# Performance work log

Measured on AMD Instinct MI355X. Metric: run time of the kernel, lower is better.

The kernel has to match this reference:

```python
import jax, jax.numpy as jnp
import numpy as np

N_NODES = 50000
N_EDGES = 800000
IN_FEATS = 128
OUT_FEATS = 128
HEADS = 2
EW_DIMS = 2
NEG_SLOPE = 0.2


def setup_inputs() -> dict:
    key = jax.random.key(0)
    ks = jax.random.split(key, 8)
    feat = jax.random.normal(ks[0], (N_NODES, IN_FEATS), dtype=jnp.float32)
    e_w = jax.random.uniform(ks[1], (N_EDGES, EW_DIMS), dtype=jnp.float32)
    src = jax.random.randint(ks[2], (N_EDGES,), 0, N_NODES)
    dst = jax.random.randint(ks[3], (N_EDGES,), 0, N_NODES)
    # Learned params: per-head fc weight, attn vectors (xavier-ish scale)
    s = 1.0 / np.sqrt(IN_FEATS)
    W = jax.random.normal(ks[4], (HEADS, OUT_FEATS, IN_FEATS), dtype=jnp.float32) * s
    attn_l = jax.random.normal(ks[5], (HEADS, OUT_FEATS), dtype=jnp.float32) * s
    attn_r = jax.random.normal(ks[6], (HEADS, OUT_FEATS), dtype=jnp.float32) * s
    attn_ew = jax.random.normal(ks[7], (HEADS, EW_DIMS), dtype=jnp.float32)
    return {"feat": feat, "e_w": e_w, "src": src, "dst": dst,
            "W": W, "attn_l": attn_l, "attn_r": attn_r, "attn_ew": attn_ew}


def reference(feat, e_w, src, dst, W, attn_l, attn_r, attn_ew):
    N = feat.shape[0]
    # per-head projection: [N, H, O]
    ft = jnp.einsum('nf,hof->nho', feat, W)
    el = jnp.einsum('nho,ho->nh', ft, attn_l)           # [N, H]
    er = jnp.einsum('nho,ho->nh', ft, attn_r)           # [N, H]
    ew = jnp.einsum('ed,hd->eh', e_w, attn_ew)          # [E, H]
    # u_add_v + edge-weight attention + leaky_relu
    e = jax.nn.leaky_relu(el[src] + er[dst] + ew, NEG_SLOPE)  # [E, H]
    # edge_softmax grouped by destination node (numerically stable)
    emax = jax.ops.segment_max(e, dst, num_segments=N)
    emax = jnp.where(jnp.isfinite(emax), emax, 0.0)
    ee = jnp.exp(e - emax[dst])
    denom = jax.ops.segment_sum(ee, dst, num_segments=N)
    a = ee / jnp.where(denom[dst] > 0, denom[dst], 1.0)       # [E, H]
    # u_mul_e / sum aggregation: [N, H, O]
    m = ft[src] * a[:, :, None]
    rst = jax.ops.segment_sum(m, dst, num_segments=N)
    # residual (Identity since in_feats == out_feats) + elu, then cat heads
    rst = jax.nn.elu(rst + feat[:, None, :])
    return rst.reshape(N, -1)
```

## Files before the change

### kernel.cpp

```cpp
#include <hip/hip_runtime.h>
#include <math.h>

#define NNODES 50000
#define NEDGES 800000
#define INF 128
#define OUTF 128
#define HEADS 2
#define NEG_SLOPE 0.2f

#define CAP 32
#define OVFCAP 32768

__device__ __forceinline__ unsigned short f2bf(float f) {
    unsigned u = __float_as_uint(f);
    unsigned r = (u + 0x7FFFu + ((u >> 16) & 1u)) >> 16;
    return (unsigned short)r;
}
__device__ __forceinline__ float bf2f(unsigned short b) {
    return __uint_as_float((unsigned)b << 16);
}

typedef __attribute__((ext_vector_type(8))) short frag_ab;
typedef __attribute__((ext_vector_type(4))) float frag_cd;

__global__ void init_kernel(int* cursor, int* ovfcnt,
                            const float* __restrict__ W,
                            const float* __restrict__ attn_l,
                            const float* __restrict__ attn_r,
                            unsigned short* __restrict__ Wb,
                            float* __restrict__ wfold, int N) {
    const int b = blockIdx.x, t = threadIdx.x;
    const int cblk = (N + 255) >> 8;
    if (b < cblk) {
        int i = b * 256 + t;
        if (i < N) cursor[i] = 0;
        if (i == 0) *ovfcnt = 0;
        return;
    }
    if (b == cblk) {
        int h = t >> 7, f = t & 127;
        float sl = 0.f, sr = 0.f;
        for (int o = 0; o < 128; ++o) {
            float wv = W[(size_t)(h * 128 + o) * 128 + f];
            sl = fmaf(attn_l[h * 128 + o], wv, sl);
            sr = fmaf(attn_r[h * 128 + o], wv, sr);
        }
        wfold[h * 128 + f] = sl;
        wfold[(2 + h) * 128 + f] = sr;
        return;
    }
    int base = (b - cblk - 1) * 4096 + t * 16;
#pragma unroll
    for (int q = 0; q < 4; ++q) {
        float4 g = *(const float4*)(W + base + q * 4);
        ushort4 v; v.x = f2bf(g.x); v.y = f2bf(g.y); v.z = f2bf(g.z); v.w = f2bf(g.w);
        *(ushort4*)(Wb + base + q * 4) = v;
    }
}

__global__ __launch_bounds__(256) void gemm_mfma(const float* __restrict__ feat,
                                                 const unsigned short* __restrict__ Wb,
                                                 const float* __restrict__ wfold,
                                                 unsigned short* __restrict__ ftb,
                                                 float* __restrict__ el,
                                                 float* __restrict__ er,
                                                 int N) {
    const int t = threadIdx.x;
    const int w = t >> 6, lane = t & 63;
    const int m16 = lane & 15, quad = lane >> 4;
    const int n0 = blockIdx.x * 64;
    const int r = n0 + w * 16 + m16;
    const bool valid = r < N;

    frag_ab af[4];
    float pd[4] = {0.f, 0.f, 0.f, 0.f};
#pragma unroll
    for (int kc = 0; kc < 4; ++kc) {
        const int cc = kc * 32 + quad * 8;
        float4 g0 = make_float4(0.f, 0.f, 0.f, 0.f), g1 = g0;
        if (valid) {
            g0 = *(const float4*)(feat + (size_t)r * INF + cc);
            g1 = *(const float4*)(feat + (size_t)r * INF + cc + 4);
        }
        frag_ab a;
        a[0] = (short)f2bf(g0.x); a[1] = (short)f2bf(g0.y);
        a[2] = (short)f2bf(g0.z); a[3] = (short)f2bf(g0.w);
        a[4] = (short)f2bf(g1.x); a[5] = (short)f2bf(g1.y);
        a[6] = (short)f2bf(g1.z); a[7] = (short)f2bf(g1.w);
        af[kc] = a;
#pragma unroll
        for (int vq = 0; vq < 4; ++vq) {
            float4 w0 = *(const float4*)(wfold + vq * 128 + cc);
            float4 w1 = *(const float4*)(wfold + vq * 128 + cc + 4);
            pd[vq] += g0.x * w0.x + g0.y * w0.y + g0.z * w0.z + g0.w * w0.w
                    + g1.x * w1.x + g1.y * w1.y + g1.z * w1.z + g1.w * w1.w;
        }
    }
#pragma unroll
    for (int m = 16; m < 64; m <<= 1)
#pragma unroll
        for (int vq = 0; vq < 4; ++vq) pd[vq] += __shfl_xor(pd[vq], m, 64);
    if (valid && quad == 0) {
        *(float2*)(el + (size_t)r * 2) = make_float2(pd[0], pd[1]);
        *(float2*)(er + (size_t)r * 2) = make_float2(pd[2], pd[3]);
    }

#pragma unroll
    for (int jt = 0; jt < 4; ++jt) {
        frag_cd acc[4];
#pragma unroll
        for (int nt = 0; nt < 4; ++nt) acc[nt] = frag_cd{0.f, 0.f, 0.f, 0.f};
#pragma unroll
        for (int kc = 0; kc < 4; ++kc) {
#pragma unroll
            for (int nt = 0; nt < 4; ++nt) {
                frag_ab bf = *(const frag_ab*)(Wb + (size_t)(jt * 64 + nt * 16 + m16) * INF
                                               + kc * 32 + quad * 8);
                acc[nt] = __builtin_amdgcn_mfma_f32_16x16x32_bf16(af[kc], bf, acc[nt], 0, 0, 0);
            }
        }
#pragma unroll
        for (int nt = 0; nt < 4; ++nt) {
            const int gj = jt * 64 + nt * 16 + m16;
#pragma unroll
            for (int reg = 0; reg < 4; ++reg) {
                int gm = n0 + w * 16 + quad * 4 + reg;
                if (gm < N) ftb[(size_t)gm * 256 + gj] = f2bf(acc[nt][reg]);
            }
        }
    }
}

__global__ void edge_fused(const float* __restrict__ el, const float* __restrict__ er,
                           const float* __restrict__ e_w, const int* __restrict__ src,
                           const int* __restrict__ dst, const float* __restrict__ attn_ew,
                           int* __restrict__ cursor, int* __restrict__ ovfcnt,
                           uint2* __restrict__ edata, float4* __restrict__ ovf,
                           int E) {
    int e = blockIdx.x * 256 + threadIdx.x;
    if (e >= E) return;
    int s = src[e], d = dst[e];
    float2 ew2 = *(const float2*)(e_w + (size_t)e * 2);
    float2 elv = *(const float2*)(el + (size_t)s * 2);
    float2 erv = *(const float2*)(er + (size_t)d * 2);
    float v0 = elv.x + erv.x + ew2.x * attn_ew[0] + ew2.y * attn_ew[1];
    float v1 = elv.y + erv.y + ew2.x * attn_ew[2] + ew2.y * attn_ew[3];
    v0 = v0 >= 0.f ? v0 : NEG_SLOPE * v0;
    v1 = v1 >= 0.f ? v1 : NEG_SLOPE * v1;
    float ee0 = __expf(v0);
    float ee1 = __expf(v1);
    int pos = atomicAdd(cursor + d, 1);
    if (pos < CAP) {
        unsigned pk = ((unsigned)f2bf(ee1) << 16) | (unsigned)f2bf(ee0);
        edata[(size_t)d * CAP + pos] = make_uint2((unsigned)s, pk);
    } else {
        int o = atomicAdd(ovfcnt, 1);
        if (o < OVFCAP)
            ovf[o] = make_float4(__int_as_float(d), __int_as_float(s), ee0, ee1);
    }
}

__global__ __launch_bounds__(256) void aggregate(const unsigned short* __restrict__ ftb,
                                                 const float* __restrict__ feat,
                                                 const uint2* __restrict__ edata,
                                                 const int* __restrict__ cursor,
                                                 const int* __restrict__ ovfcnt,
                                                 const float4* __restrict__ ovf,
                                                 float* __restrict__ out, int N) {
    const int t = threadIdx.x;
    const int w = t >> 6, l = t & 63;
    const int n = blockIdx.x * 4 + w;
    if (n >= N) return;
    const int c0 = 4 * l;
    const int h = l >> 5;
    const int cnt = cursor[n];
    const int cmain = cnt < CAP ? cnt : CAP;
    const uint2* eb = edata + (size_t)n * CAP;
    const uint2 myrec = eb[l & 31];

    float4 acc = make_float4(0.f, 0.f, 0.f, 0.f);
    float dn = 0.f;
#pragma unroll 4
    for (int i = 0; i < cmain; ++i) {
        unsigned sx = (unsigned)__builtin_amdgcn_readlane((int)myrec.x, i);
        unsigned pk = (unsigned)__builtin_amdgcn_readlane((int)myrec.y, i);
        float a = bf2f((unsigned short)(h ? (pk >> 16) : (pk & 0xFFFFu)));
        const ushort4 v = *(const ushort4*)(ftb + (size_t)sx * 256 + c0);
        dn += a;
        acc.x = fmaf(a, bf2f(v.x), acc.x);
        acc.y = fmaf(a, bf2f(v.y), acc.y);
        acc.z = fmaf(a, bf2f(v.z), acc.z);
        acc.w = fmaf(a, bf2f(v.w), acc.w);
    }
    if (cnt > CAP) {
        int no = *ovfcnt; if (no > OVFCAP) no = OVFCAP;
        for (int i = 0; i < no; ++i) {
            float4 ov = ovf[i];
            if (__float_as_int(ov.x) == n) {
                int s = __float_as_int(ov.y);
                float a = h ? ov.w : ov.z;
                dn += a;
                const ushort4 v = *(const ushort4*)(ftb + (size_t)s * 256 + c0);
                acc.x = fmaf(a, bf2f(v.x), acc.x);
                acc.y = fmaf(a, bf2f(v.y), acc.y);
                acc.z = fmaf(a, bf2f(v.z), acc.z);
                acc.w = fmaf(a, bf2f(v.w), acc.w);
            }
        }
    }
    float inv = dn > 0.f ? 1.0f / dn : 0.f;
    float4 f4 = *(const float4*)(feat + (size_t)n * INF + (c0 & 127));
    float4 r;
    r.x = acc.x * inv + f4.x;
    r.y = acc.y * inv + f4.y;
    r.z = acc.z * inv + f4.z;
    r.w = acc.w * inv + f4.w;
    r.x = r.x > 0.f ? r.x : expm1f(r.x);
    r.y = r.y > 0.f ? r.y : expm1f(r.y);
    r.z = r.z > 0.f ? r.z : expm1f(r.z);
    r.w = r.w > 0.f ? r.w : expm1f(r.w);
    *(float4*)(out + (size_t)n * 256 + c0) = r;
}

extern "C" void kernel_launch(void* const* d_in, const int* in_sizes, int n_in,
                              void* d_out, int out_size, void* d_ws, size_t ws_size,
                              hipStream_t stream) {
    const float* feat    = (const float*)d_in[0];
    const float* e_w     = (const float*)d_in[1];
    const int*   src     = (const int*)d_in[2];
    const int*   dst     = (const int*)d_in[3];
    const float* W       = (const float*)d_in[4];
    const float* attn_l  = (const float*)d_in[5];
    const float* attn_r  = (const float*)d_in[6];
    const float* attn_ew = (const float*)d_in[7];
    float* out = (float*)d_out;

    const int N = in_sizes[0] / INF;
    const int E = in_sizes[2];

    unsigned short* ftb = (unsigned short*)d_ws;
    uint2*  edata  = (uint2*)(ftb + (size_t)N * 256);
    float*  el     = (float*)(edata + (size_t)N * CAP);
    float*  er     = el + (size_t)N * 2;
    float*  wfold  = er + (size_t)N * 2;
    unsigned short* Wb = (unsigned short*)(wfold + 512);
    float4* ovf    = (float4*)(Wb + 32768);
    int*    cursor = (int*)(ovf + OVFCAP);
    int*    ovfcnt = cursor + N;

    const int cblk = (N + 255) / 256;
    init_kernel<<<cblk + 9, 256, 0, stream>>>(cursor, ovfcnt, W, attn_l, attn_r, Wb, wfold, N);

    gemm_mfma<<<(N + 63) / 64, 256, 0, stream>>>(feat, Wb, wfold, ftb, el, er, N);

    edge_fused<<<(E + 255) / 256, 256, 0, stream>>>(el, er, e_w, src, dst, attn_ew,
                                                    cursor, ovfcnt, edata, ovf, E);

    aggregate<<<(N + 3) / 4, 256, 0, stream>>>(ftb, feat, edata, cursor, ovfcnt, ovf, out, N);
}
```

Baseline: 251.3 us.

## Split aggregation edges across half-waves with 16-byte feature loads

```diff
diff --git a/kernel.cpp b/kernel.cpp
--- a/kernel.cpp
+++ b/kernel.cpp
@@ -22,6 +22,7 @@
 
 typedef __attribute__((ext_vector_type(8))) short frag_ab;
 typedef __attribute__((ext_vector_type(4))) float frag_cd;
+typedef __attribute__((ext_vector_type(8))) unsigned short ushort8v;
 
 __global__ void init_kernel(int* cursor, int* ovfcnt,
                             const float* __restrict__ W,
@@ -40,6 +41,7 @@
     if (b == cblk) {
         int h = t >> 7, f = t & 127;
         float sl = 0.f, sr = 0.f;
+#pragma unroll 16
         for (int o = 0; o < 128; ++o) {
             float wv = W[(size_t)(h * 128 + o) * 128 + f];
             sl = fmaf(attn_l[h * 128 + o], wv, sl);
@@ -105,20 +107,25 @@
         *(float2*)(er + (size_t)r * 2) = make_float2(pd[2], pd[3]);
     }
 
-#pragma unroll
+#pragma unroll 1
     for (int jt = 0; jt < 4; ++jt) {
+        frag_ab bfr[16];
+#pragma unroll
+        for (int kc = 0; kc < 4; ++kc)
+#pragma unroll
+            for (int nt = 0; nt < 4; ++nt)
+                bfr[kc * 4 + nt] = *(const frag_ab*)(Wb
+                        + (size_t)(jt * 64 + nt * 16 + m16) * INF + kc * 32 + quad * 8);
+
         frag_cd acc[4];
 #pragma unroll
         for (int nt = 0; nt < 4; ++nt) acc[nt] = frag_cd{0.f, 0.f, 0.f, 0.f};
 #pragma unroll
-        for (int kc = 0; kc < 4; ++kc) {
-#pragma unroll
-            for (int nt = 0; nt < 4; ++nt) {
-                frag_ab bf = *(const frag_ab*)(Wb + (size_t)(jt * 64 + nt * 16 + m16) * INF
-                                               + kc * 32 + quad * 8);
-                acc[nt] = __builtin_amdgcn_mfma_f32_16x16x32_bf16(af[kc], bf, acc[nt], 0, 0, 0);
-            }
-        }
+        for (int kc = 0; kc < 4; ++kc)
+#pragma unroll
+            for (int nt = 0; nt < 4; ++nt)
+                acc[nt] = __builtin_amdgcn_mfma_f32_16x16x32_bf16(af[kc], bfr[kc * 4 + nt],
+                                                                  acc[nt], 0, 0, 0);
 #pragma unroll
         for (int nt = 0; nt < 4; ++nt) {
             const int gj = jt * 64 + nt * 16 + m16;
@@ -171,27 +178,47 @@
     const int w = t >> 6, l = t & 63;
     const int n = blockIdx.x * 4 + w;
     if (n >= N) return;
-    const int c0 = 4 * l;
-    const int h = l >> 5;
+    const int hl = l & 31;
+    const int half = l >> 5;
+    const int c8 = 8 * hl;
+    const int h = hl >> 4;
     const int cnt = cursor[n];
     const int cmain = cnt < CAP ? cnt : CAP;
     const uint2* eb = edata + (size_t)n * CAP;
-    const uint2 myrec = eb[l & 31];
-
-    float4 acc = make_float4(0.f, 0.f, 0.f, 0.f);
+
+    float4 a0 = make_float4(0.f, 0.f, 0.f, 0.f);
+    float4 a1 = make_float4(0.f, 0.f, 0.f, 0.f);
     float dn = 0.f;
+    const int hm = (cmain + 1) >> 1;
 #pragma unroll 4
-    for (int i = 0; i < cmain; ++i) {
-        unsigned sx = (unsigned)__builtin_amdgcn_readlane((int)myrec.x, i);
-        unsigned pk = (unsigned)__builtin_amdgcn_readlane((int)myrec.y, i);
-        float a = bf2f((unsigned short)(h ? (pk >> 16) : (pk & 0xFFFFu)));
-        const ushort4 v = *(const ushort4*)(ftb + (size_t)sx * 256 + c0);
+    for (int i = 0; i < hm; ++i) {
+        const int j = 2 * i + half;
+        const bool vld = j < cmain;
+        uint2 rec = eb[vld ? j : 0];
+        float aw = bf2f((unsigned short)(h ? (rec.y >> 16) : (rec.y & 0xFFFFu)));
+        float a = vld ? aw : 0.f;
+        unsigned su = vld ? rec.x : 0u;
+        ushort8v v = *(const ushort8v*)(ftb + (size_t)su * 256 + c8);
         dn += a;
-        acc.x = fmaf(a, bf2f(v.x), acc.x);
-        acc.y = fmaf(a, bf2f(v.y), acc.y);
-        acc.z = fmaf(a, bf2f(v.z), acc.z);
-        acc.w = fmaf(a, bf2f(v.w), acc.w);
-    }
+        a0.x = fmaf(a, bf2f(v[0]), a0.x);
+        a0.y = fmaf(a, bf2f(v[1]), a0.y);
+        a0.z = fmaf(a, bf2f(v[2]), a0.z);
+        a0.w = fmaf(a, bf2f(v[3]), a0.w);
+        a1.x = fmaf(a, bf2f(v[4]), a1.x);
+        a1.y = fmaf(a, bf2f(v[5]), a1.y);
+        a1.z = fmaf(a, bf2f(v[6]), a1.z);
+        a1.w = fmaf(a, bf2f(v[7]), a1.w);
+    }
+    a0.x += __shfl_xor(a0.x, 32, 64);
+    a0.y += __shfl_xor(a0.y, 32, 64);
+    a0.z += __shfl_xor(a0.z, 32, 64);
+    a0.w += __shfl_xor(a0.w, 32, 64);
+    a1.x += __shfl_xor(a1.x, 32, 64);
+    a1.y += __shfl_xor(a1.y, 32, 64);
+    a1.z += __shfl_xor(a1.z, 32, 64);
+    a1.w += __shfl_xor(a1.w, 32, 64);
+    dn += __shfl_xor(dn, 32, 64);
+
     if (cnt > CAP) {
         int no = *ovfcnt; if (no > OVFCAP) no = OVFCAP;
         for (int i = 0; i < no; ++i) {
@@ -200,26 +227,32 @@
                 int s = __float_as_int(ov.y);
                 float a = h ? ov.w : ov.z;
                 dn += a;
-                const ushort4 v = *(const ushort4*)(ftb + (size_t)s * 256 + c0);
-                acc.x = fmaf(a, bf2f(v.x), acc.x);
-                acc.y = fmaf(a, bf2f(v.y), acc.y);
-                acc.z = fmaf(a, bf2f(v.z), acc.z);
-                acc.w = fmaf(a, bf2f(v.w), acc.w);
+                ushort8v v = *(const ushort8v*)(ftb + (size_t)s * 256 + c8);
+                a0.x = fmaf(a, bf2f(v[0]), a0.x);
+                a0.y = fmaf(a, bf2f(v[1]), a0.y);
+                a0.z = fmaf(a, bf2f(v[2]), a0.z);
+                a0.w = fmaf(a, bf2f(v[3]), a0.w);
+                a1.x = fmaf(a, bf2f(v[4]), a1.x);
+                a1.y = fmaf(a, bf2f(v[5]), a1.y);
+                a1.z = fmaf(a, bf2f(v[6]), a1.z);
+                a1.w = fmaf(a, bf2f(v[7]), a1.w);
             }
         }
     }
     float inv = dn > 0.f ? 1.0f / dn : 0.f;
-    float4 f4 = *(const float4*)(feat + (size_t)n * INF + (c0 & 127));
+    const int cb = c8 + 4 * half;
+    float4 av = half ? a1 : a0;
+    float4 f4 = *(const float4*)(feat + (size_t)n * INF + (cb & 127));
     float4 r;
-    r.x = acc.x * inv + f4.x;
-    r.y = acc.y * inv + f4.y;
-    r.z = acc.z * inv + f4.z;
-    r.w = acc.w * inv + f4.w;
+    r.x = fmaf(av.x, inv, f4.x);
+    r.y = fmaf(av.y, inv, f4.y);
+    r.z = fmaf(av.z, inv, f4.z);
+    r.w = fmaf(av.w, inv, f4.w);
     r.x = r.x > 0.f ? r.x : expm1f(r.x);
     r.y = r.y > 0.f ? r.y : expm1f(r.y);
     r.z = r.z > 0.f ? r.z : expm1f(r.z);
     r.w = r.w > 0.f ? r.w : expm1f(r.w);
-    *(float4*)(out + (size_t)n * 256 + c0) = r;
+    *(float4*)(out + (size_t)n * 256 + cb) = r;
 }
 
 extern "C" void kernel_launch(void* const* d_in, const int* in_sizes, int n_in,
```

Result: faster. 241.4 us (-3.9%).

## Fuse GEMM with edge scatter in warp-specialized kernel, stage W in LDS

Applied to the files above, without the earlier changes.

```diff
diff --git a/kernel.cpp b/kernel.cpp
--- a/kernel.cpp
+++ b/kernel.cpp
@@ -19,27 +19,28 @@
 __device__ __forceinline__ float bf2f(unsigned short b) {
     return __uint_as_float((unsigned)b << 16);
 }
+__device__ __forceinline__ unsigned cvt_pk_bf16(float lo, float hi) {
+    unsigned r;
+    asm("v_cvt_pk_bf16_f32 %0, %1, %2" : "=v"(r) : "v"(lo), "v"(hi));
+    return r;
+}
 
 typedef __attribute__((ext_vector_type(8))) short frag_ab;
 typedef __attribute__((ext_vector_type(4))) float frag_cd;
-
-__global__ void init_kernel(int* cursor, int* ovfcnt,
-                            const float* __restrict__ W,
+typedef __attribute__((ext_vector_type(8))) unsigned short ushort8v;
+
+#define APITCH 136
+
+__global__ void init_kernel(const float* __restrict__ W,
                             const float* __restrict__ attn_l,
                             const float* __restrict__ attn_r,
                             unsigned short* __restrict__ Wb,
-                            float* __restrict__ wfold, int N) {
+                            float* __restrict__ wfold) {
     const int b = blockIdx.x, t = threadIdx.x;
-    const int cblk = (N + 255) >> 8;
-    if (b < cblk) {
-        int i = b * 256 + t;
-        if (i < N) cursor[i] = 0;
-        if (i == 0) *ovfcnt = 0;
-        return;
-    }
-    if (b == cblk) {
+    if (b == 0) {
         int h = t >> 7, f = t & 127;
         float sl = 0.f, sr = 0.f;
+#pragma unroll 16
         for (int o = 0; o < 128; ++o) {
             float wv = W[(size_t)(h * 128 + o) * 128 + f];
             sl = fmaf(attn_l[h * 128 + o], wv, sl);
@@ -49,7 +50,7 @@
         wfold[(2 + h) * 128 + f] = sr;
         return;
     }
-    int base = (b - cblk - 1) * 4096 + t * 16;
+    int base = (b - 1) * 4096 + t * 16;
 #pragma unroll
     for (int q = 0; q < 4; ++q) {
         float4 g = *(const float4*)(W + base + q * 4);
@@ -58,105 +59,148 @@
     }
 }
 
-__global__ __launch_bounds__(256) void gemm_mfma(const float* __restrict__ feat,
-                                                 const unsigned short* __restrict__ Wb,
-                                                 const float* __restrict__ wfold,
-                                                 unsigned short* __restrict__ ftb,
-                                                 float* __restrict__ el,
-                                                 float* __restrict__ er,
-                                                 int N) {
+__global__ __launch_bounds__(256) void prep_kernel(const float* __restrict__ feat,
+                                                   const float* __restrict__ wfold,
+                                                   float* __restrict__ el,
+                                                   float* __restrict__ er,
+                                                   int* __restrict__ cursor,
+                                                   int* __restrict__ ovfcnt, int N) {
     const int t = threadIdx.x;
-    const int w = t >> 6, lane = t & 63;
+    const int gtid = blockIdx.x * 256 + t;
+    if (gtid < N) cursor[gtid] = 0;
+    if (gtid == 0) *ovfcnt = 0;
+    const int lid = t & 31;
+    const int n = blockIdx.x * 8 + (t >> 5);
+    if (n >= N) return;
+    float4 f4 = *(const float4*)(feat + (size_t)n * INF + lid * 4);
+    float pd[4];
+#pragma unroll
+    for (int vq = 0; vq < 4; ++vq) {
+        float4 wv = *(const float4*)(wfold + vq * 128 + lid * 4);
+        pd[vq] = f4.x * wv.x + f4.y * wv.y + f4.z * wv.z + f4.w * wv.w;
+    }
+#pragma unroll
+    for (int m = 1; m < 32; m <<= 1)
+#pragma unroll
+        for (int vq = 0; vq < 4; ++vq) pd[vq] += __shfl_xor(pd[vq], m, 64);
+    if (lid == 0) {
+        *(float2*)(el + (size_t)n * 2) = make_float2(pd[0], pd[1]);
+        *(float2*)(er + (size_t)n * 2) = make_float2(pd[2], pd[3]);
+    }
+}
+
+__global__ __launch_bounds__(512) void fused_gemm_edge(
+        const float* __restrict__ feat, const unsigned short* __restrict__ Wb,
+        unsigned short* __restrict__ ftb,
+        const float* __restrict__ el, const float* __restrict__ er,
+        const float* __restrict__ e_w, const int* __restrict__ src,
+        const int* __restrict__ dst, const float* __restrict__ attn_ew,
+        int* __restrict__ cursor, int* __restrict__ ovfcnt,
+        uint2* __restrict__ edata, float4* __restrict__ ovf,
+        int N, int E) {
+    __shared__ unsigned short Bs[256 * APITCH];
+    const int t = threadIdx.x;
+    const int lane = t & 63;
     const int m16 = lane & 15, quad = lane >> 4;
-    const int n0 = blockIdx.x * 64;
-    const int r = n0 + w * 16 + m16;
-    const bool valid = r < N;
-
-    frag_ab af[4];
-    float pd[4] = {0.f, 0.f, 0.f, 0.f};
-#pragma unroll
-    for (int kc = 0; kc < 4; ++kc) {
-        const int cc = kc * 32 + quad * 8;
-        float4 g0 = make_float4(0.f, 0.f, 0.f, 0.f), g1 = g0;
-        if (valid) {
-            g0 = *(const float4*)(feat + (size_t)r * INF + cc);
-            g1 = *(const float4*)(feat + (size_t)r * INF + cc + 4);
-        }
-        frag_ab a;
-        a[0] = (short)f2bf(g0.x); a[1] = (short)f2bf(g0.y);
-        a[2] = (short)f2bf(g0.z); a[3] = (short)f2bf(g0.w);
-        a[4] = (short)f2bf(g1.x); a[5] = (short)f2bf(g1.y);
-        a[6] = (short)f2bf(g1.z); a[7] = (short)f2bf(g1.w);
-        af[kc] = a;
-#pragma unroll
-        for (int vq = 0; vq < 4; ++vq) {
-            float4 w0 = *(const float4*)(wfold + vq * 128 + cc);
-            float4 w1 = *(const float4*)(wfold + vq * 128 + cc + 4);
-            pd[vq] += g0.x * w0.x + g0.y * w0.y + g0.z * w0.z + g0.w * w0.w
-                    + g1.x * w1.x + g1.y * w1.y + g1.z * w1.z + g1.w * w1.w;
-        }
-    }
-#pragma unroll
-    for (int m = 16; m < 64; m <<= 1)
-#pragma unroll
-        for (int vq = 0; vq < 4; ++vq) pd[vq] += __shfl_xor(pd[vq], m, 64);
-    if (valid && quad == 0) {
-        *(float2*)(el + (size_t)r * 2) = make_float2(pd[0], pd[1]);
-        *(float2*)(er + (size_t)r * 2) = make_float2(pd[2], pd[3]);
-    }
-
-#pragma unroll
-    for (int jt = 0; jt < 4; ++jt) {
-        frag_cd acc[4];
-#pragma unroll
-        for (int nt = 0; nt < 4; ++nt) acc[nt] = frag_cd{0.f, 0.f, 0.f, 0.f};
+    const int n0 = blockIdx.x * 128;
+
+    frag_ab af[2][4];
+    bool vr0 = false, vr1 = false;
+    int r0n = 0, r1n = 0;
+    if (t < 256) {
+        const int w = t >> 6;
+        r0n = n0 + w * 16 + m16;
+        r1n = r0n + 64;
+        vr0 = r0n < N; vr1 = r1n < N;
 #pragma unroll
         for (int kc = 0; kc < 4; ++kc) {
-#pragma unroll
-            for (int nt = 0; nt < 4; ++nt) {
-                frag_ab bf = *(const frag_ab*)(Wb + (size_t)(jt * 64 + nt * 16 + m16) * INF
-                                               + kc * 32 + quad * 8);
-                acc[nt] = __builtin_amdgcn_mfma_f32_16x16x32_bf16(af[kc], bf, acc[nt], 0, 0, 0);
-            }
-        }
-#pragma unroll
-        for (int nt = 0; nt < 4; ++nt) {
-            const int gj = jt * 64 + nt * 16 + m16;
-#pragma unroll
-            for (int reg = 0; reg < 4; ++reg) {
-                int gm = n0 + w * 16 + quad * 4 + reg;
-                if (gm < N) ftb[(size_t)gm * 256 + gj] = f2bf(acc[nt][reg]);
-            }
-        }
-    }
-}
-
-__global__ void edge_fused(const float* __restrict__ el, const float* __restrict__ er,
-                           const float* __restrict__ e_w, const int* __restrict__ src,
-                           const int* __restrict__ dst, const float* __restrict__ attn_ew,
-                           int* __restrict__ cursor, int* __restrict__ ovfcnt,
-                           uint2* __restrict__ edata, float4* __restrict__ ovf,
-                           int E) {
-    int e = blockIdx.x * 256 + threadIdx.x;
-    if (e >= E) return;
-    int s = src[e], d = dst[e];
-    float2 ew2 = *(const float2*)(e_w + (size_t)e * 2);
-    float2 elv = *(const float2*)(el + (size_t)s * 2);
-    float2 erv = *(const float2*)(er + (size_t)d * 2);
-    float v0 = elv.x + erv.x + ew2.x * attn_ew[0] + ew2.y * attn_ew[1];
-    float v1 = elv.y + erv.y + ew2.x * attn_ew[2] + ew2.y * attn_ew[3];
-    v0 = v0 >= 0.f ? v0 : NEG_SLOPE * v0;
-    v1 = v1 >= 0.f ? v1 : NEG_SLOPE * v1;
-    float ee0 = __expf(v0);
-    float ee1 = __expf(v1);
-    int pos = atomicAdd(cursor + d, 1);
-    if (pos < CAP) {
-        unsigned pk = ((unsigned)f2bf(ee1) << 16) | (unsigned)f2bf(ee0);
-        edata[(size_t)d * CAP + pos] = make_uint2((unsigned)s, pk);
+            const int cc = kc * 32 + quad * 8;
+            float4 ga0 = make_float4(0.f, 0.f, 0.f, 0.f), ga1 = ga0;
+            float4 gb0 = ga0, gb1 = ga0;
+            if (vr0) {
+                ga0 = *(const float4*)(feat + (size_t)r0n * INF + cc);
+                ga1 = *(const float4*)(feat + (size_t)r0n * INF + cc + 4);
+            }
+            if (vr1) {
+                gb0 = *(const float4*)(feat + (size_t)r1n * INF + cc);
+                gb1 = *(const float4*)(feat + (size_t)r1n * INF + cc + 4);
+            }
+            union { int4 i; frag_ab f; } ua, ub;
+            ua.i.x = (int)cvt_pk_bf16(ga0.x, ga0.y); ua.i.y = (int)cvt_pk_bf16(ga0.z, ga0.w);
+            ua.i.z = (int)cvt_pk_bf16(ga1.x, ga1.y); ua.i.w = (int)cvt_pk_bf16(ga1.z, ga1.w);
+            ub.i.x = (int)cvt_pk_bf16(gb0.x, gb0.y); ub.i.y = (int)cvt_pk_bf16(gb0.z, gb0.w);
+            ub.i.z = (int)cvt_pk_bf16(gb1.x, gb1.y); ub.i.w = (int)cvt_pk_bf16(gb1.z, gb1.w);
+            af[0][kc] = ua.f; af[1][kc] = ub.f;
+        }
+    }
+
+#pragma unroll
+    for (int i = 0; i < 8; ++i) {
+        int q = t + i * 512;
+        int row = q >> 4, c = q & 15;
+        ushort8v v = *(const ushort8v*)(Wb + row * 128 + c * 8);
+        *(ushort8v*)(&Bs[row * APITCH + c * 8]) = v;
+    }
+    __syncthreads();
+
+    if (t < 256) {
+#pragma unroll 1
+        for (int jt = 0; jt < 4; ++jt) {
+            frag_cd acc[2][4];
+#pragma unroll
+            for (int rg = 0; rg < 2; ++rg)
+#pragma unroll
+                for (int nt = 0; nt < 4; ++nt) acc[rg][nt] = frag_cd{0.f, 0.f, 0.f, 0.f};
+#pragma unroll
+            for (int kc = 0; kc < 4; ++kc)
+#pragma unroll
+                for (int nt = 0; nt < 4; ++nt) {
+                    frag_ab bf = *(const frag_ab*)(&Bs[(jt * 64 + nt * 16 + m16) * APITCH
+                                                       + kc * 32 + quad * 8]);
+                    acc[0][nt] = __builtin_amdgcn_mfma_f32_16x16x32_bf16(bf, af[0][kc],
+                                                                         acc[0][nt], 0, 0, 0);
+                    acc[1][nt] = __builtin_amdgcn_mfma_f32_16x16x32_bf16(bf, af[1][kc],
+                                                                         acc[1][nt], 0, 0, 0);
+                }
+#pragma unroll
+            for (int rg = 0; rg < 2; ++rg) {
+                const int rr = rg ? r1n : r0n;
+                if (rg ? vr1 : vr0) {
+#pragma unroll
+                    for (int nt = 0; nt < 4; ++nt) {
+                        uint2 p;
+                        p.x = cvt_pk_bf16(acc[rg][nt][0], acc[rg][nt][1]);
+                        p.y = cvt_pk_bf16(acc[rg][nt][2], acc[rg][nt][3]);
+                        *(uint2*)(ftb + (size_t)rr * 256 + jt * 64 + nt * 16 + quad * 4) = p;
+                    }
+                }
+            }
+        }
     } else {
-        int o = atomicAdd(ovfcnt, 1);
-        if (o < OVFCAP)
-            ovf[o] = make_float4(__int_as_float(d), __int_as_float(s), ee0, ee1);
+        const float aew0 = attn_ew[0], aew1 = attn_ew[1];
+        const float aew2 = attn_ew[2], aew3 = attn_ew[3];
+        const int stride = gridDim.x * 256;
+        for (int e = blockIdx.x * 256 + (t - 256); e < E; e += stride) {
+            int s = src[e], d = dst[e];
+            float2 ew2 = *(const float2*)(e_w + (size_t)e * 2);
+            float2 elv = *(const float2*)(el + (size_t)s * 2);
+            float2 erv = *(const float2*)(er + (size_t)d * 2);
+            float v0 = elv.x + erv.x + ew2.x * aew0 + ew2.y * aew1;
+            float v1 = elv.y + erv.y + ew2.x * aew2 + ew2.y * aew3;
+            v0 = v0 >= 0.f ? v0 : NEG_SLOPE * v0;
+            v1 = v1 >= 0.f ? v1 : NEG_SLOPE * v1;
+            float ee0 = __expf(v0);
+            float ee1 = __expf(v1);
+            int pos = atomicAdd(cursor + d, 1);
+            if (pos < CAP) {
+                unsigned pk = ((unsigned)f2bf(ee1) << 16) | (unsigned)f2bf(ee0);
+                edata[(size_t)d * CAP + pos] = make_uint2((unsigned)s, pk);
+            } else {
+                int o = atomicAdd(ovfcnt, 1);
+                if (o < OVFCAP)
+                    ovf[o] = make_float4(__int_as_float(d), __int_as_float(s), ee0, ee1);
+            }
+        }
     }
 }
 
@@ -176,21 +220,20 @@
     const int cnt = cursor[n];
     const int cmain = cnt < CAP ? cnt : CAP;
     const uint2* eb = edata + (size_t)n * CAP;
-    const uint2 myrec = eb[l & 31];
 
     float4 acc = make_float4(0.f, 0.f, 0.f, 0.f);
     float dn = 0.f;
 #pragma unroll 4
     for (int i = 0; i < cmain; ++i) {
-        unsigned sx = (unsigned)__builtin_amdgcn_readlane((int)myrec.x, i);
-        unsigned pk = (unsigned)__builtin_amdgcn_readlane((int)myrec.y, i);
-        float a = bf2f((unsigned short)(h ? (pk >> 16) : (pk & 0xFFFFu)));
-        const ushort4 v = *(const ushort4*)(ftb + (size_t)sx * 256 + c0);
+        uint2 rec = eb[i];
+        int s = (int)rec.x;
+        float a = bf2f((unsigned short)(h ? (rec.y >> 16) : (rec.y & 0xFFFFu)));
         dn += a;
-        acc.x = fmaf(a, bf2f(v.x), acc.x);
-        acc.y = fmaf(a, bf2f(v.y), acc.y);
-        acc.z = fmaf(a, bf2f(v.z), acc.z);
-        acc.w = fmaf(a, bf2f(v.w), acc.w);
+        ushort4 v = *(const ushort4*)(ftb + (size_t)s * 256 + c0);
+        acc.x += a * bf2f(v.x);
+        acc.y += a * bf2f(v.y);
+        acc.z += a * bf2f(v.z);
+        acc.w += a * bf2f(v.w);
     }
     if (cnt > CAP) {
         int no = *ovfcnt; if (no > OVFCAP) no = OVFCAP;
@@ -200,11 +243,11 @@
                 int s = __float_as_int(ov.y);
                 float a = h ? ov.w : ov.z;
                 dn += a;
-                const ushort4 v = *(const ushort4*)(ftb + (size_t)s * 256 + c0);
-                acc.x = fmaf(a, bf2f(v.x), acc.x);
-                acc.y = fmaf(a, bf2f(v.y), acc.y);
-                acc.z = fmaf(a, bf2f(v.z), acc.z);
-                acc.w = fmaf(a, bf2f(v.w), acc.w);
+                ushort4 v = *(const ushort4*)(ftb + (size_t)s * 256 + c0);
+                acc.x += a * bf2f(v.x);
+                acc.y += a * bf2f(v.y);
+                acc.z += a * bf2f(v.z);
+                acc.w += a * bf2f(v.w);
             }
         }
     }
@@ -248,13 +291,13 @@
     int*    cursor = (int*)(ovf + OVFCAP);
     int*    ovfcnt = cursor + N;
 
-    const int cblk = (N + 255) / 256;
-    init_kernel<<<cblk + 9, 256, 0, stream>>>(cursor, ovfcnt, W, attn_l, attn_r, Wb, wfold, N);
-
-    gemm_mfma<<<(N + 63) / 64, 256, 0, stream>>>(feat, Wb, wfold, ftb, el, er, N);
-
-    edge_fused<<<(E + 255) / 256, 256, 0, stream>>>(el, er, e_w, src, dst, attn_ew,
-                                                    cursor, ovfcnt, edata, ovf, E);
+    init_kernel<<<9, 256, 0, stream>>>(W, attn_l, attn_r, Wb, wfold);
+
+    prep_kernel<<<(N + 7) / 8, 256, 0, stream>>>(feat, wfold, el, er, cursor, ovfcnt, N);
+
+    fused_gemm_edge<<<(N + 127) / 128, 512, 0, stream>>>(feat, Wb, ftb, el, er, e_w,
+                                                         src, dst, attn_ew,
+                                                         cursor, ovfcnt, edata, ovf, N, E);
 
     aggregate<<<(N + 3) / 4, 256, 0, stream>>>(ftb, feat, edata, cursor, ovfcnt, ovf, out, N);
 }
```

Result: faster. 214.6 us (-14.6%).
